# Kernel optimization log

Hardware: AMD Instinct MI355X
Metric: run time of the kernel (lower is better)

Reference implementation:

```python
import jax, jax.numpy as jnp
import numpy as np

N_NODES = 100000
F_DIM = 128      # graph.num_node_features
TE_DIM = 32      # te_emb_dim
D = F_DIM + TE_DIM  # attention embed_dim = 160
B = 4096         # number of target nodes (batched python loop)
K = 64           # candidates per target
TAU = 1.0
THRESHOLD = 0.2
EPS = 1e-10


def setup_inputs() -> dict:
    key = jax.random.key(0)
    ks = jax.random.split(key, 16)
    inp = {
        "x": jax.random.normal(ks[0], (N_NODES, F_DIM), dtype=jnp.float32),
        "target_node_ids": jax.random.randint(ks[1], (B,), 0, N_NODES),
        "target_node_times": jax.random.randint(ks[2], (B,), 1, 10000),
        "neighbor_ids": jax.random.randint(ks[3], (B, K), 0, N_NODES),
        "edge_time": jax.random.randint(ks[4], (B, K), 0, 10000),
        "edge_weight": jax.random.uniform(ks[5], (B, K), dtype=jnp.float32),
        "gumbel_u": jax.random.uniform(ks[6], (B, K), dtype=jnp.float32),
        # TemporalEncoding params: te(t) = cos(t * w + b)
        "te_w": jax.random.normal(ks[7], (TE_DIM,), dtype=jnp.float32),
        "te_b": jax.random.normal(ks[8], (TE_DIM,), dtype=jnp.float32),
        # MultiheadAttention params (packed qkv like torch)
        "in_proj_w": jax.random.normal(ks[9], (3 * D, D), dtype=jnp.float32) / np.sqrt(D),
        "in_proj_b": jnp.zeros((3 * D,), dtype=jnp.float32),
        "out_w": jax.random.normal(ks[10], (D, D), dtype=jnp.float32) / np.sqrt(D),
        "out_b": jnp.zeros((D,), dtype=jnp.float32),
        # MLP: Linear(D+1 -> 1) + LeakyReLU
        "mlp_w": jax.random.normal(ks[11], (D + 1,), dtype=jnp.float32) / np.sqrt(D + 1),
        "mlp_b": jnp.zeros((1,), dtype=jnp.float32),
    }
    return inp


def reference(x, target_node_ids, target_node_times, neighbor_ids, edge_time,
              edge_weight, gumbel_u, te_w, te_b, in_proj_w, in_proj_b,
              out_w, out_b, mlp_w, mlp_b):
    # --- build target embedding: [B, D]
    t_x = x[target_node_ids]                                          # [B, F]
    t_te = jnp.cos(target_node_times[:, None].astype(jnp.float32) * te_w + te_b)  # [B, TE]
    q_in = jnp.concatenate([t_x, t_te], axis=-1)                      # [B, D]

    # --- candidate embeddings: [B, K, D]
    c_x = x[neighbor_ids]                                             # [B, K, F]
    c_te = jnp.cos(edge_time[..., None].astype(jnp.float32) * te_w + te_b)        # [B, K, TE]
    kv_in = jnp.concatenate([c_x, c_te], axis=-1)                     # [B, K, D]

    # --- single-head MultiheadAttention (eval mode, 1 query per target)
    Wq, Wk, Wv = in_proj_w[:D], in_proj_w[D:2 * D], in_proj_w[2 * D:]
    bq, bk, bv = in_proj_b[:D], in_proj_b[D:2 * D], in_proj_b[2 * D:]
    q = q_in @ Wq.T + bq                                              # [B, D]
    k = jnp.einsum('bkf,df->bkd', kv_in, Wk) + bk                     # [B, K, D]
    v = jnp.einsum('bkf,df->bkd', kv_in, Wv) + bv                     # [B, K, D]
    scores = jnp.einsum('bd,bkd->bk', q, k) / jnp.sqrt(jnp.float32(D))
    attn_w = jax.nn.softmax(scores, axis=-1)                          # [B, K]
    ctx = jnp.einsum('bk,bkd->bd', attn_w, v)                         # [B, D]
    attn_output = ctx @ out_w.T + out_b                               # [B, D]

    # --- gumbel-softmax mask over attention weights (soft, then threshold)
    g = -jnp.log(-jnp.log(gumbel_u + EPS) + EPS)                      # gumbel(0,1)
    y_soft = jax.nn.softmax((attn_w + g) / TAU, axis=-1)
    candidate_mask = y_soft > THRESHOLD                               # [B, K] bool

    # --- MLP edge-weight update: Linear(D+1 -> 1) + LeakyReLU
    mlp_in = jnp.concatenate(
        [jnp.broadcast_to(attn_output[:, None, :], (attn_output.shape[0], edge_weight.shape[1], attn_output.shape[1])),
         edge_weight[..., None]], axis=-1)                            # [B, K, D+1]
    new_edge_weight = jax.nn.leaky_relu(jnp.einsum('bkf,f->bk', mlp_in, mlp_w) + mlp_b[0])  # [B, K]

    return attn_output, new_edge_weight, candidate_mask
```

## Files before the change

kernel.cpp:

```cpp
#include <hip/hip_runtime.h>

#define F_DIM 128
#define TE_DIM 32
#define DD 160
#define NB 4096
#define KK 64

#define WS_M    0
#define WS_V2   25600
#define WS_C    51200
#define WS_U    51360
#define WS_B2   51520
#define WS_S0   51680
#define WS_WTOT 51681
#define WS_QT   51712
#define WS_SBK  707072
#define WS_WKV  711168

__device__ __forceinline__ float dot4acc(const float4 w, const float4 v, float a) {
    a = fmaf(w.x, v.x, a);
    a = fmaf(w.y, v.y, a);
    a = fmaf(w.z, v.z, a);
    a = fmaf(w.w, v.w, a);
    return a;
}
__device__ __forceinline__ float wave_max(float v) {
    #pragma unroll
    for (int off = 32; off > 0; off >>= 1) v = fmaxf(v, __shfl_xor(v, off, 64));
    return v;
}
__device__ __forceinline__ float wave_sum(float v) {
    #pragma unroll
    for (int off = 32; off > 0; off >>= 1) v += __shfl_xor(v, off, 64);
    return v;
}

__global__ void setup_kernel(const float* __restrict__ ipw, const float* __restrict__ ipb,
                             const float* __restrict__ ow,  const float* __restrict__ ob,
                             float* __restrict__ ws)
{
    const int g = blockIdx.x * blockDim.x + threadIdx.x;
    const float inv = 0.07905694150420949f;
    if (g < 25600) {
        const int e = g / DD, f = g % DD;
        const float* wk = ipw + DD * DD;
        float a = 0.f;
        for (int d = 0; d < DD; ++d) a = fmaf(wk[d * DD + e], ipw[d * DD + f], a);
        ws[WS_M + g] = a * inv;
    } else if (g < 51200) {
        const int gg = g - 25600;
        const int i = gg / DD, f = gg % DD;
        const float* wv = ipw + 2 * DD * DD;
        float a = 0.f;
        for (int d = 0; d < DD; ++d) a = fmaf(ow[i * DD + d], wv[d * DD + f], a);
        ws[WS_V2 + gg] = a;
    } else if (g < 51360) {
        const int e = g - 51200;
        const float* wk = ipw + DD * DD;
        float a = 0.f;
        for (int d = 0; d < DD; ++d) a = fmaf(wk[d * DD + e], ipb[d], a);
        ws[WS_C + e] = a * inv;
    } else if (g < 51520) {
        const int f = g - 51360;
        float a = 0.f;
        for (int d = 0; d < DD; ++d) a = fmaf(ipw[d * DD + f], ipb[DD + d], a);
        ws[WS_U + f] = a * inv;
    } else if (g < 51680) {
        const int i = g - 51520;
        float a = ob[i];
        for (int d = 0; d < DD; ++d) a = fmaf(ow[i * DD + d], ipb[2 * DD + d], a);
        ws[WS_B2 + i] = a;
    } else if (g == 51680) {
        float a = 0.f;
        for (int d = 0; d < DD; ++d) a = fmaf(ipb[d], ipb[DD + d], a);
        ws[WS_S0] = a * inv;
    }
}

__global__ __launch_bounds__(256)
void qt_kernel(const float* __restrict__ x,
               const int* __restrict__ tni, const int* __restrict__ tnt,
               const float* __restrict__ te_w, const float* __restrict__ te_b,
               float* __restrict__ ws)
{
    __shared__ __attribute__((aligned(16))) float s_qin[16][164];
    __shared__ int   s_tn[16];
    __shared__ float s_tt[16];
    const int t  = threadIdx.x;
    const int b0 = blockIdx.x * 16;

    if (t < 16) { s_tn[t] = tni[b0 + t]; s_tt[t] = (float)tnt[b0 + t]; }
    __syncthreads();

    {
        const int r = t >> 4, seg = t & 15;
        const float4* src = (const float4*)(x + (long)s_tn[r] * F_DIM + seg * 8);
        const float4 a = src[0], bq = src[1];
        *(float4*)&s_qin[r][seg * 8]     = a;
        *(float4*)&s_qin[r][seg * 8 + 4] = bq;
        const int j2 = seg * 2;
        s_qin[r][F_DIM + j2]     = cosf(s_tt[r] * te_w[j2]     + te_b[j2]);
        s_qin[r][F_DIM + j2 + 1] = cosf(s_tt[r] * te_w[j2 + 1] + te_b[j2 + 1]);
    }
    __syncthreads();

    {
        const int r = t >> 4, seg = t & 15;
        const float* U = ws + WS_U;
        float p = 0.f;
        #pragma unroll
        for (int i = 0; i < 10; ++i) p = fmaf(s_qin[r][seg * 10 + i], U[seg * 10 + i], p);
        #pragma unroll
        for (int off = 1; off < 16; off <<= 1) p += __shfl_xor(p, off, 64);
        if (seg == 0) ws[WS_SBK + b0 + r] = p + ws[WS_S0];
    }

    {
        const int r = t & 15, eg = t >> 4;
        const float* M = ws + WS_M;
        const float* C = ws + WS_C;
        float acc[10];
        #pragma unroll
        for (int j = 0; j < 10; ++j) acc[j] = C[eg * 10 + j];
        for (int f0 = 0; f0 < DD; f0 += 8) {
            const float4 q0 = *(const float4*)&s_qin[r][f0];
            const float4 q1 = *(const float4*)&s_qin[r][f0 + 4];
            #pragma unroll
            for (int j = 0; j < 10; ++j) {
                const float4* mp = (const float4*)(M + (long)(eg * 10 + j) * DD + f0);
                acc[j] = dot4acc(mp[0], q0, acc[j]);
                acc[j] = dot4acc(mp[1], q1, acc[j]);
            }
        }
        float* qt = ws + WS_QT + (long)(b0 + r) * DD + eg * 10;
        #pragma unroll
        for (int j = 0; j < 10; ++j) qt[j] = acc[j];
    }
}

__global__ __launch_bounds__(256, 4)
void attn_kernel(const float* __restrict__ x,
                 const int* __restrict__ neighbor_ids,
                 const int* __restrict__ edge_time,
                 const float* __restrict__ gumbel_u,
                 const float* __restrict__ te_w, const float* __restrict__ te_b,
                 float* __restrict__ ws,
                 float* __restrict__ out_mask)
{
    __shared__ __attribute__((aligned(4))) _Float16 s_te[4][KK][36];
    __shared__ int   s_nid[4][KK];
    __shared__ float s_sc[4][KK];
    __shared__ float s_aw[4][KK];
    __shared__ float s_qte[4][TE_DIM];

    const int tid = threadIdx.x, wr = tid >> 6, lane = tid & 63;
    const long b = (long)blockIdx.x * 4 + wr;

    {
        s_nid[wr][lane] = neighbor_ids[b * KK + lane];
        const float etv = (float)edge_time[b * KK + lane];
        #pragma unroll
        for (int jj = 0; jj < 16; ++jj) {
            union { _Float16 h[2]; unsigned u; } pk;
            pk.h[0] = (_Float16)cosf(etv * te_w[2 * jj]     + te_b[2 * jj]);
            pk.h[1] = (_Float16)cosf(etv * te_w[2 * jj + 1] + te_b[2 * jj + 1]);
            *(unsigned*)&s_te[wr][lane][2 * jj] = pk.u;
        }
    }
    const int fl = lane & 31, half = lane >> 5;
    const float4 qf = *(const float4*)(ws + WS_QT + b * DD + 4 * fl);
    if (lane < TE_DIM) s_qte[wr][lane] = ws[WS_QT + b * DD + F_DIM + lane];
    const float sbk = ws[WS_SBK + b];

    float tedot = 0.f;
    #pragma unroll
    for (int jj = 0; jj < 16; ++jj) {
        union { _Float16 h[2]; unsigned u; } pk;
        pk.u = *(const unsigned*)&s_te[wr][lane][2 * jj];
        tedot = fmaf(s_qte[wr][2 * jj],     (float)pk.h[0], tedot);
        tedot = fmaf(s_qte[wr][2 * jj + 1], (float)pk.h[1], tedot);
    }

    #pragma unroll 4
    for (int i = 0; i < 32; ++i) {
        const int k  = 2 * i + half;
        const int nk = s_nid[wr][k];
        const float4 xv = *(const float4*)(x + (long)nk * F_DIM + 4 * fl);
        float p = 0.f;
        p = dot4acc(xv, qf, p);
        p += __shfl_xor(p, 16, 64);
        p += __shfl_xor(p, 8, 64);
        p += __shfl_xor(p, 4, 64);
        p += __shfl_xor(p, 2, 64);
        p += __shfl_xor(p, 1, 64);
        if (fl == 0) s_sc[wr][k] = p;
    }

    float aw;
    {
        const float sc = s_sc[wr][lane] + tedot + sbk;
        const float m = wave_max(sc);
        const float e = expf(sc - m);
        const float l = wave_sum(e);
        aw = e / l;
        s_aw[wr][lane] = aw;
    }

    {
        const float u = gumbel_u[b * KK + lane];
        const float g = -logf(-logf(u + 1e-10f) + 1e-10f);
        const float z = aw + g;
        const float m = wave_max(z);
        const float e = expf(z - m);
        const float l = wave_sum(e);
        out_mask[b * KK + lane] = (e / l > 0.2f) ? 1.0f : 0.0f;
    }

    {
        float ax = 0.f, ay = 0.f, at = 0.f;
        const float* xb = x + lane * 2;
        const int lte = lane & 31;
        #pragma unroll 8
        for (int k = 0; k < KK; ++k) {
            const float wgt = s_aw[wr][k];
            const int   nk  = s_nid[wr][k];
            const float2 xv = *(const float2*)(xb + (long)nk * F_DIM);
            ax = fmaf(wgt, xv.x, ax);
            ay = fmaf(wgt, xv.y, ay);
            at = fmaf(wgt, (float)s_te[wr][k][lte], at);
        }
        float* wkv = ws + WS_WKV + b * DD;
        wkv[lane * 2]     = ax;
        wkv[lane * 2 + 1] = ay;
        if (lane < TE_DIM) wkv[F_DIM + lane] = at;
    }
}

__global__ __launch_bounds__(256)
void ao_kernel(const float* __restrict__ edge_weight,
               const float* __restrict__ mlp_w, const float* __restrict__ mlp_b,
               float* __restrict__ ws,
               float* __restrict__ out_ao, float* __restrict__ out_new)
{
    __shared__ __attribute__((aligned(16))) float s_v[16][164];
    __shared__ __attribute__((aligned(16))) float s_ao[16][164];
    __shared__ float s_base[16];
    const int t  = threadIdx.x;
    const int b0 = blockIdx.x * 16;

    #pragma unroll
    for (int c = 0; c < 10; ++c) {
        const int idx = t + 256 * c;
        s_v[idx / DD][idx % DD] = ws[WS_WKV + (long)b0 * DD + idx];
    }
    __syncthreads();

    {
        const int r = t & 15, eg = t >> 4;
        const float* V2 = ws + WS_V2;
        const float* B2 = ws + WS_B2;
        float acc[10];
        #pragma unroll
        for (int j = 0; j < 10; ++j) acc[j] = B2[eg * 10 + j];
        for (int f0 = 0; f0 < DD; f0 += 8) {
            const float4 q0 = *(const float4*)&s_v[r][f0];
            const float4 q1 = *(const float4*)&s_v[r][f0 + 4];
            #pragma unroll
            for (int j = 0; j < 10; ++j) {
                const float4* mp = (const float4*)(V2 + (long)(eg * 10 + j) * DD + f0);
                acc[j] = dot4acc(mp[0], q0, acc[j]);
                acc[j] = dot4acc(mp[1], q1, acc[j]);
            }
        }
        #pragma unroll
        for (int j = 0; j < 10; ++j) s_ao[r][eg * 10 + j] = acc[j];
    }
    __syncthreads();

    {
        const int r = t >> 4, seg = t & 15;
        float p = 0.f;
        #pragma unroll
        for (int i = 0; i < 10; ++i) p = fmaf(s_ao[r][seg * 10 + i], mlp_w[seg * 10 + i], p);
        #pragma unroll
        for (int off = 1; off < 16; off <<= 1) p += __shfl_xor(p, off, 64);
        if (seg == 0) s_base[r] = p + mlp_b[0];
    }
    __syncthreads();

    #pragma unroll
    for (int c = 0; c < 10; ++c) {
        const int idx = t + 256 * c;
        out_ao[(long)b0 * DD + idx] = s_ao[idx / DD][idx % DD];
    }
    #pragma unroll
    for (int c = 0; c < 4; ++c) {
        const int idx = t + 256 * c;
        const int r = idx >> 6, kx = idx & 63;
        const float ew  = edge_weight[(long)(b0 + r) * KK + kx];
        const float val = fmaf(ew, mlp_w[DD], s_base[r]);
        out_new[(long)(b0 + r) * KK + kx] = (val >= 0.f) ? val : 0.01f * val;
    }
}

extern "C" void kernel_launch(void* const* d_in, const int* in_sizes, int n_in,
                              void* d_out, int out_size, void* d_ws, size_t ws_size,
                              hipStream_t stream) {
    const float* x   = (const float*)d_in[0];
    const int*   tni = (const int*)d_in[1];
    const int*   tnt = (const int*)d_in[2];
    const int*   nid = (const int*)d_in[3];
    const int*   et  = (const int*)d_in[4];
    const float* ew  = (const float*)d_in[5];
    const float* gu  = (const float*)d_in[6];
    const float* tew = (const float*)d_in[7];
    const float* teb = (const float*)d_in[8];
    const float* ipw = (const float*)d_in[9];
    const float* ipb = (const float*)d_in[10];
    const float* ow  = (const float*)d_in[11];
    const float* ob  = (const float*)d_in[12];
    const float* mw  = (const float*)d_in[13];
    const float* mb  = (const float*)d_in[14];

    float* wsf = (float*)d_ws;

    float* out      = (float*)d_out;
    float* out_ao   = out;
    float* out_new  = out + (long)NB * DD;
    float* out_mask = out + (long)NB * DD + (long)NB * KK;

    setup_kernel<<<(WS_WTOT + 255) / 256, 256, 0, stream>>>(ipw, ipb, ow, ob, wsf);
    qt_kernel<<<NB / 16, 256, 0, stream>>>(x, tni, tnt, tew, teb, wsf);
    attn_kernel<<<NB / 4, 256, 0, stream>>>(x, nid, et, gu, tew, teb, wsf, out_mask);
    ao_kernel<<<NB / 16, 256, 0, stream>>>(ew, mw, mb, wsf, out_ao, out_new);
}
```

Measured before the change: 195.1 us.

## Stage gathered neighbor rows in LDS as fp16 and split each target across two waves

The attention kernel now keeps each gathered neighbor feature row in shared memory as fp16 during the score pass. The weighted-sum pass reads from that copy instead of gathering x from global memory a second time. Each target is now handled by two waves, each covering half the candidates, and the partial sums are combined through shared memory, so a block covers two targets instead of four. This removes the second global gather but adds block-wide barriers and rounds the context accumulation inputs to fp16.

```diff
diff --git a/kernel.cpp b/kernel.cpp
--- a/kernel.cpp
+++ b/kernel.cpp
@@ -5,6 +5,9 @@
 #define DD 160
 #define NB 4096
 #define KK 64
+#define TPB 2
+#define XR_STRIDE 132
+#define TE_STRIDE 34
 
 #define WS_M    0
 #define WS_V2   25600
@@ -16,6 +19,9 @@
 #define WS_QT   51712
 #define WS_SBK  707072
 #define WS_WKV  711168
+
+typedef _Float16 half4_t __attribute__((ext_vector_type(4)));
+typedef _Float16 half2_t __attribute__((ext_vector_type(2)));
 
 __device__ __forceinline__ float dot4acc(const float4 w, const float4 v, float a) {
     a = fmaf(w.x, v.x, a);
@@ -147,66 +153,79 @@
                  float* __restrict__ ws,
                  float* __restrict__ out_mask)
 {
-    __shared__ __attribute__((aligned(4))) _Float16 s_te[4][KK][36];
-    __shared__ int   s_nid[4][KK];
-    __shared__ float s_sc[4][KK];
-    __shared__ float s_aw[4][KK];
-    __shared__ float s_qte[4][TE_DIM];
-
-    const int tid = threadIdx.x, wr = tid >> 6, lane = tid & 63;
-    const long b = (long)blockIdx.x * 4 + wr;
-
-    {
-        s_nid[wr][lane] = neighbor_ids[b * KK + lane];
-        const float etv = (float)edge_time[b * KK + lane];
-        #pragma unroll
-        for (int jj = 0; jj < 16; ++jj) {
-            union { _Float16 h[2]; unsigned u; } pk;
-            pk.h[0] = (_Float16)cosf(etv * te_w[2 * jj]     + te_b[2 * jj]);
-            pk.h[1] = (_Float16)cosf(etv * te_w[2 * jj + 1] + te_b[2 * jj + 1]);
-            *(unsigned*)&s_te[wr][lane][2 * jj] = pk.u;
-        }
-    }
-    const int fl = lane & 31, half = lane >> 5;
+    __shared__ __attribute__((aligned(16))) _Float16 s_xrow[TPB][KK][XR_STRIDE];
+    __shared__ __attribute__((aligned(4)))  _Float16 s_te[TPB][KK][TE_STRIDE];
+    __shared__ int   s_nid[TPB][KK];
+    __shared__ float s_sc[TPB][KK];
+    __shared__ float s_aw[TPB][KK];
+    __shared__ float s_qte[TPB][TE_DIM];
+    __shared__ float s_wp[TPB][2][DD];
+
+    const int tid  = threadIdx.x;
+    const int w    = tid >> 6;
+    const int lane = tid & 63;
+    const int t    = w >> 1;
+    const int h    = w & 1;
+    const long b   = (long)blockIdx.x * TPB + t;
+
+    {
+        if (lane < 32) s_nid[t][32 * h + lane] = neighbor_ids[b * KK + 32 * h + lane];
+        const int kl   = 32 * h + (lane >> 1);
+        const int side = lane & 1;
+        const float etv = (float)edge_time[b * KK + kl];
+        #pragma unroll
+        for (int q = 0; q < 8; ++q) {
+            const int jj = 8 * side + q;
+            union { _Float16 hh[2]; unsigned u; } pk;
+            pk.hh[0] = (_Float16)cosf(etv * te_w[2 * jj]     + te_b[2 * jj]);
+            pk.hh[1] = (_Float16)cosf(etv * te_w[2 * jj + 1] + te_b[2 * jj + 1]);
+            *(unsigned*)&s_te[t][kl][2 * jj] = pk.u;
+        }
+        if (h == 0 && lane < TE_DIM) s_qte[t][lane] = ws[WS_QT + b * DD + F_DIM + lane];
+    }
+
+    const int fl = lane & 31, h2 = lane >> 5;
     const float4 qf = *(const float4*)(ws + WS_QT + b * DD + 4 * fl);
-    if (lane < TE_DIM) s_qte[wr][lane] = ws[WS_QT + b * DD + F_DIM + lane];
     const float sbk = ws[WS_SBK + b];
 
-    float tedot = 0.f;
-    #pragma unroll
-    for (int jj = 0; jj < 16; ++jj) {
-        union { _Float16 h[2]; unsigned u; } pk;
-        pk.u = *(const unsigned*)&s_te[wr][lane][2 * jj];
-        tedot = fmaf(s_qte[wr][2 * jj],     (float)pk.h[0], tedot);
-        tedot = fmaf(s_qte[wr][2 * jj + 1], (float)pk.h[1], tedot);
-    }
-
     #pragma unroll 4
-    for (int i = 0; i < 32; ++i) {
-        const int k  = 2 * i + half;
-        const int nk = s_nid[wr][k];
+    for (int i = 0; i < 16; ++i) {
+        const int k  = 32 * h + 2 * i + h2;
+        const int nk = s_nid[t][k];
         const float4 xv = *(const float4*)(x + (long)nk * F_DIM + 4 * fl);
-        float p = 0.f;
-        p = dot4acc(xv, qf, p);
+        half4_t hv;
+        hv.x = (_Float16)xv.x; hv.y = (_Float16)xv.y;
+        hv.z = (_Float16)xv.z; hv.w = (_Float16)xv.w;
+        *(half4_t*)&s_xrow[t][k][4 * fl] = hv;
+        float p = dot4acc(xv, qf, 0.f);
         p += __shfl_xor(p, 16, 64);
         p += __shfl_xor(p, 8, 64);
         p += __shfl_xor(p, 4, 64);
         p += __shfl_xor(p, 2, 64);
         p += __shfl_xor(p, 1, 64);
-        if (fl == 0) s_sc[wr][k] = p;
-    }
+        if (fl == 0) s_sc[t][k] = p;
+    }
+    __syncthreads();
 
     float aw;
     {
-        const float sc = s_sc[wr][lane] + tedot + sbk;
+        float tedot = 0.f;
+        #pragma unroll
+        for (int jj = 0; jj < 16; ++jj) {
+            union { _Float16 hh[2]; unsigned u; } pk;
+            pk.u = *(const unsigned*)&s_te[t][lane][2 * jj];
+            tedot = fmaf(s_qte[t][2 * jj],     (float)pk.hh[0], tedot);
+            tedot = fmaf(s_qte[t][2 * jj + 1], (float)pk.hh[1], tedot);
+        }
+        const float sc = s_sc[t][lane] + tedot + sbk;
         const float m = wave_max(sc);
         const float e = expf(sc - m);
         const float l = wave_sum(e);
         aw = e / l;
-        s_aw[wr][lane] = aw;
-    }
-
-    {
+        if (h == 0) s_aw[t][lane] = aw;
+    }
+
+    if (h == 0) {
         const float u = gumbel_u[b * KK + lane];
         const float g = -logf(-logf(u + 1e-10f) + 1e-10f);
         const float z = aw + g;
@@ -215,24 +234,32 @@
         const float l = wave_sum(e);
         out_mask[b * KK + lane] = (e / l > 0.2f) ? 1.0f : 0.0f;
     }
+    __syncthreads();
 
     {
         float ax = 0.f, ay = 0.f, at = 0.f;
-        const float* xb = x + lane * 2;
         const int lte = lane & 31;
         #pragma unroll 8
-        for (int k = 0; k < KK; ++k) {
-            const float wgt = s_aw[wr][k];
-            const int   nk  = s_nid[wr][k];
-            const float2 xv = *(const float2*)(xb + (long)nk * F_DIM);
-            ax = fmaf(wgt, xv.x, ax);
-            ay = fmaf(wgt, xv.y, ay);
-            at = fmaf(wgt, (float)s_te[wr][k][lte], at);
-        }
+        for (int kk = 0; kk < 32; ++kk) {
+            const int k = 32 * h + kk;
+            const float wgt = s_aw[t][k];
+            const half2_t hp = *(const half2_t*)&s_xrow[t][k][2 * lane];
+            ax = fmaf(wgt, (float)hp.x, ax);
+            ay = fmaf(wgt, (float)hp.y, ay);
+            at = fmaf(wgt, (float)s_te[t][k][lte], at);
+        }
+        s_wp[t][h][2 * lane]     = ax;
+        s_wp[t][h][2 * lane + 1] = ay;
+        if (lane < TE_DIM) s_wp[t][h][F_DIM + lane] = at;
+    }
+    __syncthreads();
+
+    if (h == 0) {
         float* wkv = ws + WS_WKV + b * DD;
-        wkv[lane * 2]     = ax;
-        wkv[lane * 2 + 1] = ay;
-        if (lane < TE_DIM) wkv[F_DIM + lane] = at;
+        wkv[lane]      = s_wp[t][0][lane]      + s_wp[t][1][lane];
+        wkv[lane + 64] = s_wp[t][0][lane + 64] + s_wp[t][1][lane + 64];
+        if (lane < 32)
+            wkv[lane + 128] = s_wp[t][0][lane + 128] + s_wp[t][1][lane + 128];
     }
 }
 
@@ -331,6 +358,6 @@
 
     setup_kernel<<<(WS_WTOT + 255) / 256, 256, 0, stream>>>(ipw, ipb, ow, ob, wsf);
     qt_kernel<<<NB / 16, 256, 0, stream>>>(x, tni, tnt, tew, teb, wsf);
-    attn_kernel<<<NB / 4, 256, 0, stream>>>(x, nid, et, gu, tew, teb, wsf, out_mask);
+    attn_kernel<<<NB / TPB, 256, 0, stream>>>(x, nid, et, gu, tew, teb, wsf, out_mask);
     ao_kernel<<<NB / 16, 256, 0, stream>>>(ew, mw, mb, wsf, out_ao, out_new);
 }
```

New measurement: 206.0 us. 1.06x slower.
